# Performance work log

Measured on AMD Instinct MI355X. Metric: run time of the kernel, lower is better.

## Reference

```python
import jax, jax.numpy as jnp
import numpy as np

N_POINTS = 500000   # collocation points
N_TERMS = 64        # library terms
N_OUT = 4           # number of outputs / equations


def setup_inputs() -> dict:
    key = jax.random.key(0)
    k1, k2 = jax.random.split(key)
    thetas = jax.random.normal(k1, (N_POINTS, N_TERMS), dtype=jnp.float32)
    # n_out time derivatives packed as columns of a single [N, n_out] array
    time_derivs = jax.random.normal(k2, (N_POINTS, N_OUT), dtype=jnp.float32)
    return {"thetas": thetas, "time_derivs": time_derivs}


def reference(thetas, time_derivs):
    # sparsity masks are all-True at init, so apply_mask is identity and all
    # n_out least-squares problems share the same (full) library matrix.
    sparse_theta = thetas  # [N, n_terms]
    xtx = thetas.T @ thetas              # [n_terms, n_terms] (shared Gram)
    xty = thetas.T @ time_derivs         # [n_terms, n_out]
    # torch.inverse(X^T X) @ (X^T y), batched over outputs as columns
    coeffs = jnp.linalg.inv(xtx) @ xty   # [n_terms, n_out]
    return (sparse_theta, coeffs)
```

## Files before the change

kernel.cpp:

```cpp
#include <hip/hip_runtime.h>

#define N_ROWS   500000
#define N_TERMS  64
#define N_OUT    4
#define CHUNK_R  32
#define NCHUNK   (N_ROWS / CHUNK_R)
#define NB       512
#define WAVES_TOTAL (NB * 4)
#define PART_STRIDE (N_TERMS * N_TERMS + N_TERMS * N_OUT)
#define CHUNKS   8
#define PER_CHUNK (NB / CHUNKS)
#define JACOBI_ITERS 20

typedef float f32x4  __attribute__((ext_vector_type(4)));
typedef short bf16x8 __attribute__((ext_vector_type(8)));

__device__ inline unsigned short f32_bf16(float f) {
  unsigned int u = __builtin_bit_cast(unsigned int, f);
  u += 0x7fffu + ((u >> 16) & 1u);
  return (unsigned short)(u >> 16);
}

__global__ __launch_bounds__(256, 3) void k1_gram(const float* __restrict__ th,
                                                  const float* __restrict__ td,
                                                  float* __restrict__ out_copy,
                                                  float* __restrict__ part) {
  const int tid  = threadIdx.x;
  const int wv   = tid >> 6;
  const int lane = tid & 63;
  const int g    = lane >> 4;
  const int l15  = lane & 15;

  f32x4 c00 = {0.f,0.f,0.f,0.f}, c01 = c00, c02 = c00, c03 = c00;
  f32x4 c11 = c00, c12 = c00, c13 = c00, c22 = c00, c23 = c00, c33 = c00;
  float accY[4][4];
#pragma unroll
  for (int i = 0; i < 4; ++i)
#pragma unroll
    for (int o = 0; o < 4; ++o) accY[i][o] = 0.f;

  const float4* td4 = (const float4*)td;

  for (int ch = blockIdx.x * 4 + wv; ch < NCHUNK; ch += WAVES_TOTAL) {
    const int r0 = ch * CHUNK_R;

    float4 yv = make_float4(0.f, 0.f, 0.f, 0.f);
    if (lane < 32) yv = td4[r0 + lane];

    const float* base = th + (size_t)(r0 + 8 * g) * 64 + l15;
    float f[4][8];
#pragma unroll
    for (int j = 0; j < 8; ++j)
#pragma unroll
      for (int i = 0; i < 4; ++i)
        f[i][j] = base[j * 64 + i * 16];

    float* ob = out_copy + (size_t)(r0 + 8 * g) * 64 + l15;
#pragma unroll
    for (int j = 0; j < 8; ++j)
#pragma unroll
      for (int i = 0; i < 4; ++i)
        __builtin_nontemporal_store(f[i][j], ob + j * 64 + i * 16);

#pragma unroll
    for (int j = 0; j < 8; ++j) {
      const int src = 8 * g + j;
      const float y0 = __shfl(yv.x, src);
      const float y1 = __shfl(yv.y, src);
      const float y2 = __shfl(yv.z, src);
      const float y3 = __shfl(yv.w, src);
#pragma unroll
      for (int i = 0; i < 4; ++i) {
        accY[i][0] += f[i][j] * y0;
        accY[i][1] += f[i][j] * y1;
        accY[i][2] += f[i][j] * y2;
        accY[i][3] += f[i][j] * y3;
      }
    }

    bf16x8 fr[4];
#pragma unroll
    for (int i = 0; i < 4; ++i)
#pragma unroll
      for (int j = 0; j < 8; ++j)
        fr[i][j] = (short)f32_bf16(f[i][j]);

    c00 = __builtin_amdgcn_mfma_f32_16x16x32_bf16(fr[0], fr[0], c00, 0, 0, 0);
    c01 = __builtin_amdgcn_mfma_f32_16x16x32_bf16(fr[0], fr[1], c01, 0, 0, 0);
    c02 = __builtin_amdgcn_mfma_f32_16x16x32_bf16(fr[0], fr[2], c02, 0, 0, 0);
    c03 = __builtin_amdgcn_mfma_f32_16x16x32_bf16(fr[0], fr[3], c03, 0, 0, 0);
    c11 = __builtin_amdgcn_mfma_f32_16x16x32_bf16(fr[1], fr[1], c11, 0, 0, 0);
    c12 = __builtin_amdgcn_mfma_f32_16x16x32_bf16(fr[1], fr[2], c12, 0, 0, 0);
    c13 = __builtin_amdgcn_mfma_f32_16x16x32_bf16(fr[1], fr[3], c13, 0, 0, 0);
    c22 = __builtin_amdgcn_mfma_f32_16x16x32_bf16(fr[2], fr[2], c22, 0, 0, 0);
    c23 = __builtin_amdgcn_mfma_f32_16x16x32_bf16(fr[2], fr[3], c23, 0, 0, 0);
    c33 = __builtin_amdgcn_mfma_f32_16x16x32_bf16(fr[3], fr[3], c33, 0, 0, 0);
  }

#pragma unroll
  for (int i = 0; i < 4; ++i)
#pragma unroll
    for (int o = 0; o < 4; ++o) {
      float v = accY[i][o];
      v += __shfl_xor(v, 16);
      v += __shfl_xor(v, 32);
      accY[i][o] = v;
    }

  __shared__ float red[64 * 65];
  __shared__ float yred[256];

  for (int w = 0; w < 4; ++w) {
    if (wv == w) {
      const bool first = (w == 0);
#define WR_TILE(A, B, C)                                                    \
  {                                                                         \
    _Pragma("unroll") for (int r = 0; r < 4; ++r) {                         \
      const int e = (16 * (A) + 4 * g + r) * 65 + 16 * (B) + l15;           \
      if (first) red[e] = (C)[r]; else red[e] += (C)[r];                    \
    }                                                                       \
  }
#define WR_TILE_T(A, B, C)                                                  \
  {                                                                         \
    _Pragma("unroll") for (int r = 0; r < 4; ++r) {                         \
      const int e = (16 * (B) + l15) * 65 + 16 * (A) + 4 * g + r;           \
      if (first) red[e] = (C)[r]; else red[e] += (C)[r];                    \
    }                                                                       \
  }
      WR_TILE(0, 0, c00);
      WR_TILE(0, 1, c01); WR_TILE_T(0, 1, c01);
      WR_TILE(0, 2, c02); WR_TILE_T(0, 2, c02);
      WR_TILE(0, 3, c03); WR_TILE_T(0, 3, c03);
      WR_TILE(1, 1, c11);
      WR_TILE(1, 2, c12); WR_TILE_T(1, 2, c12);
      WR_TILE(1, 3, c13); WR_TILE_T(1, 3, c13);
      WR_TILE(2, 2, c22);
      WR_TILE(2, 3, c23); WR_TILE_T(2, 3, c23);
      WR_TILE(3, 3, c33);
#undef WR_TILE
#undef WR_TILE_T
      if (g == 0) {
#pragma unroll
        for (int i = 0; i < 4; ++i)
#pragma unroll
          for (int o = 0; o < 4; ++o) {
            const int e = (16 * i + l15) * 4 + o;
            if (first) yred[e] = accY[i][o]; else yred[e] += accY[i][o];
          }
      }
    }
    __syncthreads();
  }

  float* p = part + blockIdx.x * PART_STRIDE;
#pragma unroll
  for (int s = 0; s < 16; ++s) {
    const int e = s * 256 + tid;
    p[e] = red[(e >> 6) * 65 + (e & 63)];
  }
  p[4096 + tid] = yred[tid];
}

__global__ __launch_bounds__(256) void k2a_reduce(const float* __restrict__ part,
                                                  float* __restrict__ mid) {
  const int eblk = blockIdx.x % 17;
  const int bch  = blockIdx.x / 17;
  const int e = eblk * 256 + threadIdx.x;
  if (e >= PART_STRIDE) return;
  const float* base = part + (size_t)bch * PER_CHUNK * PART_STRIDE + e;
  float s = 0.f;
  for (int i = 0; i < PER_CHUNK; ++i) s += base[i * PART_STRIDE];
  mid[bch * PART_STRIDE + e] = s;
}

__global__ __launch_bounds__(256) void k3_solve(const float* __restrict__ mid,
                                                float* __restrict__ coef_out) {
  __shared__ float A[64 * 65];
  __shared__ float bX[64 * 4];
  __shared__ float X0[64 * 4];
  __shared__ float X1[64 * 4];
  const int tid = threadIdx.x;

#pragma unroll
  for (int s = 0; s < 17; ++s) {
    const int e = s * 256 + tid;
    if (e < PART_STRIDE) {
      float v = 0.f;
#pragma unroll
      for (int c = 0; c < CHUNKS; ++c) v += mid[c * PART_STRIDE + e];
      if (e < 4096) A[(e >> 6) * 65 + (e & 63)] = v;
      else          bX[e - 4096] = v;
    }
  }
  __syncthreads();

  const int i = tid >> 2;
  const int c = tid & 3;

  float arow[64];
#pragma unroll
  for (int j = 0; j < 64; ++j) arow[j] = A[i * 65 + j];

  const float dinv = 1.0f / A[i * 65 + i];
  const float b = bX[i * 4 + c];

  float x0 = b * dinv;
  X0[tid] = x0;
  __syncthreads();

  float xlast = x0;
  for (int it = 0; it < JACOBI_ITERS; ++it) {
    const float* Xr = (it & 1) ? X1 : X0;
    float*       Xw = (it & 1) ? X0 : X1;
    float s0 = 0.f, s1 = 0.f, s2 = 0.f, s3 = 0.f;
#pragma unroll
    for (int j = 0; j < 64; j += 4) {
      s0 += arow[j]     * Xr[(j)     * 4 + c];
      s1 += arow[j + 1] * Xr[(j + 1) * 4 + c];
      s2 += arow[j + 2] * Xr[(j + 2) * 4 + c];
      s3 += arow[j + 3] * Xr[(j + 3) * 4 + c];
    }
    const float s = (s0 + s1) + (s2 + s3);
    xlast = xlast + (b - s) * dinv;
    Xw[tid] = xlast;
    __syncthreads();
  }

  coef_out[tid] = xlast;
}

extern "C" void kernel_launch(void* const* d_in, const int* in_sizes, int n_in,
                              void* d_out, int out_size, void* d_ws, size_t ws_size,
                              hipStream_t stream) {
  const float* th = (const float*)d_in[0];
  const float* td = (const float*)d_in[1];
  float* out = (float*)d_out;
  float* ws  = (float*)d_ws;

  float* part = ws;
  float* mid  = ws + (size_t)NB * PART_STRIDE;

  hipLaunchKernelGGL(k1_gram, dim3(NB), dim3(256), 0, stream, th, td, out, part);
  hipLaunchKernelGGL(k2a_reduce, dim3(17 * CHUNKS), dim3(256), 0, stream, part, mid);
  hipLaunchKernelGGL(k3_solve, dim3(1), dim3(256), 0, stream, mid,
                     out + (size_t)N_ROWS * N_TERMS);
}
```

Baseline: 80.63 us.

## Stage theta chunks through swizzled LDS with float4 loads, 8 waves per block

Each wave now loads its 32x64 chunk with coalesced float4 loads and writes the output copy with plain float4 stores. It stages the chunk into an XOR-swizzled per-wave LDS tile and builds the bf16 MFMA fragments and the X^T y products from that tile. Blocks grow to 512 threads (8 waves), and the LDS staging buffer is reused for the final reduction. The aim is to replace strided scalar global loads and nontemporal stores with wide coalesced accesses. The cost is extra LDS traffic per chunk and a longer serial per-wave reduction, and it drops the nontemporal hint on the copy.

```diff
diff --git a/kernel.cpp b/kernel.cpp
--- a/kernel.cpp
+++ b/kernel.cpp
@@ -6,14 +6,15 @@
 #define CHUNK_R  32
 #define NCHUNK   (N_ROWS / CHUNK_R)
 #define NB       512
-#define WAVES_TOTAL (NB * 4)
+#define WAVES_PB 8
+#define WAVES_TOTAL (NB * WAVES_PB)
 #define PART_STRIDE (N_TERMS * N_TERMS + N_TERMS * N_OUT)
 #define CHUNKS   8
 #define PER_CHUNK (NB / CHUNKS)
 #define JACOBI_ITERS 20
 
-typedef float f32x4  __attribute__((ext_vector_type(4)));
-typedef short bf16x8 __attribute__((ext_vector_type(8)));
+typedef float f32x4   __attribute__((ext_vector_type(4)));
+typedef short bf16x8  __attribute__((ext_vector_type(8)));
 
 __device__ inline unsigned short f32_bf16(float f) {
   unsigned int u = __builtin_bit_cast(unsigned int, f);
@@ -21,69 +22,64 @@
   return (unsigned short)(u >> 16);
 }
 
-__global__ __launch_bounds__(256, 3) void k1_gram(const float* __restrict__ th,
+__device__ inline bf16x8 frag_col(const float* __restrict__ Tf, int cswz, int k0) {
+  bf16x8 r;
+#pragma unroll
+  for (int j = 0; j < 8; ++j)
+    r[j] = (short)f32_bf16(Tf[(k0 + j) * 64 + cswz]);
+  return r;
+}
+
+__global__ __launch_bounds__(512, 4) void k1_gram(const float* __restrict__ th,
                                                   const float* __restrict__ td,
                                                   float* __restrict__ out_copy,
                                                   float* __restrict__ part) {
+  __shared__ float4 W4[WAVES_PB * 544];
+
   const int tid  = threadIdx.x;
   const int wv   = tid >> 6;
   const int lane = tid & 63;
   const int g    = lane >> 4;
   const int l15  = lane & 15;
+  const int kg   = g * 8;
+  const int szf  = (g & 1) << 4;
+
+  float4* Wt = W4 + wv * 544;
+  float4* Wy = Wt + 512;
+  const float* Tf = (const float*)Wt;
 
   f32x4 c00 = {0.f,0.f,0.f,0.f}, c01 = c00, c02 = c00, c03 = c00;
   f32x4 c11 = c00, c12 = c00, c13 = c00, c22 = c00, c23 = c00, c33 = c00;
-  float accY[4][4];
-#pragma unroll
-  for (int i = 0; i < 4; ++i)
-#pragma unroll
-    for (int o = 0; o < 4; ++o) accY[i][o] = 0.f;
-
+  float accY[4] = {0.f, 0.f, 0.f, 0.f};
+
+  const float4* th4 = (const float4*)th;
   const float4* td4 = (const float4*)td;
-
-  for (int ch = blockIdx.x * 4 + wv; ch < NCHUNK; ch += WAVES_TOTAL) {
-    const int r0 = ch * CHUNK_R;
-
+  float4* out4 = (float4*)out_copy;
+
+  for (int ch = blockIdx.x * WAVES_PB + wv; ch < NCHUNK; ch += WAVES_TOTAL) {
+    const size_t r0 = (size_t)ch * CHUNK_R;
+    const float4* src = th4 + r0 * 16;
+    float4*       dst = out4 + r0 * 16;
+
+    float4 cur[8];
+#pragma unroll
+    for (int j = 0; j < 8; ++j) cur[j] = src[j * 64 + lane];
     float4 yv = make_float4(0.f, 0.f, 0.f, 0.f);
     if (lane < 32) yv = td4[r0 + lane];
 
-    const float* base = th + (size_t)(r0 + 8 * g) * 64 + l15;
-    float f[4][8];
-#pragma unroll
-    for (int j = 0; j < 8; ++j)
-#pragma unroll
-      for (int i = 0; i < 4; ++i)
-        f[i][j] = base[j * 64 + i * 16];
-
-    float* ob = out_copy + (size_t)(r0 + 8 * g) * 64 + l15;
-#pragma unroll
-    for (int j = 0; j < 8; ++j)
-#pragma unroll
-      for (int i = 0; i < 4; ++i)
-        __builtin_nontemporal_store(f[i][j], ob + j * 64 + i * 16);
-
 #pragma unroll
     for (int j = 0; j < 8; ++j) {
-      const int src = 8 * g + j;
-      const float y0 = __shfl(yv.x, src);
-      const float y1 = __shfl(yv.y, src);
-      const float y2 = __shfl(yv.z, src);
-      const float y3 = __shfl(yv.w, src);
-#pragma unroll
-      for (int i = 0; i < 4; ++i) {
-        accY[i][0] += f[i][j] * y0;
-        accY[i][1] += f[i][j] * y1;
-        accY[i][2] += f[i][j] * y2;
-        accY[i][3] += f[i][j] * y3;
-      }
-    }
+      dst[j * 64 + lane] = cur[j];
+      const int fi  = j * 64 + lane;
+      const int swz = ((fi >> 7) & 1) << 2;
+      Wt[(fi & ~15) | ((fi & 15) ^ swz)] = cur[j];
+    }
+    if (lane < 32) Wy[lane] = yv;
 
     bf16x8 fr[4];
 #pragma unroll
     for (int i = 0; i < 4; ++i)
-#pragma unroll
-      for (int j = 0; j < 8; ++j)
-        fr[i][j] = (short)f32_bf16(f[i][j]);
+      fr[i] = frag_col(Tf, (16 * i + l15) ^ szf, kg);
 
     c00 = __builtin_amdgcn_mfma_f32_16x16x32_bf16(fr[0], fr[0], c00, 0, 0, 0);
     c01 = __builtin_amdgcn_mfma_f32_16x16x32_bf16(fr[0], fr[1], c01, 0, 0, 0);
@@ -95,22 +91,24 @@
     c22 = __builtin_amdgcn_mfma_f32_16x16x32_bf16(fr[2], fr[2], c22, 0, 0, 0);
     c23 = __builtin_amdgcn_mfma_f32_16x16x32_bf16(fr[2], fr[3], c23, 0, 0, 0);
     c33 = __builtin_amdgcn_mfma_f32_16x16x32_bf16(fr[3], fr[3], c33, 0, 0, 0);
-  }
-
-#pragma unroll
-  for (int i = 0; i < 4; ++i)
-#pragma unroll
-    for (int o = 0; o < 4; ++o) {
-      float v = accY[i][o];
-      v += __shfl_xor(v, 16);
-      v += __shfl_xor(v, 32);
-      accY[i][o] = v;
-    }
-
-  __shared__ float red[64 * 65];
-  __shared__ float yred[256];
-
-  for (int w = 0; w < 4; ++w) {
+
+#pragma unroll
+    for (int r = 0; r < CHUNK_R; ++r) {
+      const int sz = ((r >> 3) & 1) << 4;
+      const float  tv = Tf[r * 64 + (lane ^ sz)];
+      const float4 yr = Wy[r];
+      accY[0] += tv * yr.x;
+      accY[1] += tv * yr.y;
+      accY[2] += tv * yr.z;
+      accY[3] += tv * yr.w;
+    }
+  }
+
+  __syncthreads();
+  float* red  = (float*)W4;
+  float* yred = red + 64 * 65;
+
+  for (int w = 0; w < WAVES_PB; ++w) {
     if (wv == w) {
       const bool first = (w == 0);
 #define WR_TILE(A, B, C)                                                    \
@@ -139,14 +137,10 @@
       WR_TILE(3, 3, c33);
 #undef WR_TILE
 #undef WR_TILE_T
-      if (g == 0) {
-#pragma unroll
-        for (int i = 0; i < 4; ++i)
-#pragma unroll
-          for (int o = 0; o < 4; ++o) {
-            const int e = (16 * i + l15) * 4 + o;
-            if (first) yred[e] = accY[i][o]; else yred[e] += accY[i][o];
-          }
+#pragma unroll
+      for (int o = 0; o < 4; ++o) {
+        const int e = lane * 4 + o;
+        if (first) yred[e] = accY[o]; else yred[e] += accY[o];
       }
     }
     __syncthreads();
@@ -154,11 +148,11 @@
 
   float* p = part + blockIdx.x * PART_STRIDE;
 #pragma unroll
-  for (int s = 0; s < 16; ++s) {
-    const int e = s * 256 + tid;
+  for (int s = 0; s < 8; ++s) {
+    const int e = s * 512 + tid;
     p[e] = red[(e >> 6) * 65 + (e & 63)];
   }
-  p[4096 + tid] = yred[tid];
+  if (tid < 256) p[4096 + tid] = yred[tid];
 }
 
 __global__ __launch_bounds__(256) void k2a_reduce(const float* __restrict__ part,
@@ -240,7 +234,7 @@
   float* part = ws;
   float* mid  = ws + (size_t)NB * PART_STRIDE;
 
-  hipLaunchKernelGGL(k1_gram, dim3(NB), dim3(256), 0, stream, th, td, out, part);
+  hipLaunchKernelGGL(k1_gram, dim3(NB), dim3(512), 0, stream, th, td, out, part);
   hipLaunchKernelGGL(k2a_reduce, dim3(17 * CHUNKS), dim3(256), 0, stream, part, mid);
   hipLaunchKernelGGL(k3_solve, dim3(1), dim3(256), 0, stream, mid,
                      out + (size_t)N_ROWS * N_TERMS);
```

After: 76.08 us. 5.6% less time.
